# Kernel optimization log

Hardware: AMD Instinct MI355X
Metric: run time of the kernel (lower is better)

## Reference

```python
import jax, jax.numpy as jnp
import numpy as np

P, L = 4, 2                      # meta-paths, sub-layers
N_NODES, N_EDGES = 100000, 1600000
E_TABLE = 200000                 # global edge-feature table rows
D_IN = D_OUT = 128
D_META, NREG = 64, 50000
SCALE = np.float32(1.0 / np.sqrt(D_OUT))


def setup_inputs() -> dict:
    key = jax.random.key(0)
    ks = jax.random.split(key, 8)
    E = jax.random.normal(ks[0], (E_TABLE, D_IN), jnp.float32)
    metapath_emb = jax.random.normal(ks[1], (P, D_META), jnp.float32)
    W_root = jax.random.normal(ks[2], (P, L, D_IN, D_OUT), jnp.float32) * 0.05
    W_rel = jax.random.normal(ks[3], (P, L, D_IN, D_OUT), jnp.float32) * 0.05
    b = jnp.zeros((P, L, D_OUT), jnp.float32)
    Wq = jax.random.normal(ks[4], (D_META, D_OUT), jnp.float32) * 0.05
    bq = jnp.zeros((D_OUT,), jnp.float32)
    edge_index = jax.random.randint(ks[5], (P, 2, N_EDGES), 0, N_NODES, dtype=jnp.int64)
    eids = jax.random.randint(ks[6], (P, N_NODES), 0, E_TABLE, dtype=jnp.int64)
    return dict(E=E, metapath_emb=metapath_emb, W_root=W_root, W_rel=W_rel, b=b,
                Wq=Wq, bq=bq, edge_index=edge_index, eids=eids)


def _rgcn(x, src, dst, Wr, Wm, bias):
    # PyG RGCNConv, single relation, mean aggregation:
    # h_i = mean_{j->i}(x_j @ Wm) + x_i @ Wr + bias
    msg = x[src] @ Wm                                           # [E, d_out]
    agg = jax.ops.segment_sum(msg, dst, num_segments=N_NODES)   # [N, d_out]
    cnt = jax.ops.segment_sum(jnp.ones((src.shape[0], 1), x.dtype), dst,
                              num_segments=N_NODES)
    return agg / jnp.maximum(cnt, 1.0) + x @ Wr + bias


def reference(E, metapath_emb, W_root, W_rel, b, Wq, bq, edge_index, eids):
    sems = []
    for i in range(P):                      # small fixed loop over meta-paths
        src, dst = edge_index[i, 0], edge_index[i, 1]
        x = E[eids[i]]                      # gather edge features, [N, d_in]
        for j in range(L):
            x = jax.nn.relu(_rgcn(x, src, dst, W_root[i, j], W_rel[i, j], b[i, j]))
        sems.append(x[:NREG])
    emb = jnp.stack(sems, axis=1)           # [NREG, P, d_out]
    query = metapath_emb @ Wq + bq          # [P, d_out]
    # bmm + diagonal extraction == per-(n,p) dot product
    scores = jnp.einsum('pd,npd->np', query, emb) * SCALE
    w = jax.nn.softmax(scores, axis=1)      # softmax over meta-paths
    return jnp.sum(w[:, :, None] * emb, axis=1)   # [NREG, d_out]
```

## Files before the change

kernel.cpp:

```cpp
#include <hip/hip_runtime.h>

#define N_NODES 100000
#define N_EDGES 1600000
#define E_TBL   200000
#define D       128
#define NREG    50000
#define P_MP    4
#define L_SUB   2
#define D_META  64
#define SCALE_F 0.08838834764831845f

#define BKT_SHIFT 9
#define BKT_NODES 512
#define NBKT      196
#define CSB       128
#define EPB       (N_EDGES / CSB)
#define P2N       (NBKT * CSB)

typedef __attribute__((ext_vector_type(8))) short bf16x8;
typedef __attribute__((ext_vector_type(4))) float f32x4;
typedef __attribute__((ext_vector_type(2))) float f32x2;


__device__ __forceinline__ float bf2f_lo(unsigned int u) {
    union { unsigned int i; float f; } v;
    v.i = u << 16;
    return v.f;
}
__device__ __forceinline__ float bf2f_hi(unsigned int u) {
    union { unsigned int i; float f; } v;
    v.i = u & 0xffff0000u;
    return v.f;
}
__device__ __forceinline__ unsigned int f2bf(float f) {
    union { float f; unsigned int i; } v;
    v.f = f;
    return (v.i + 0x7fffu + ((v.i >> 16) & 1u)) >> 16;
}


__global__ __launch_bounds__(256) void p1_bhist(const int* __restrict__ edge_index,
                                                int* __restrict__ tbl) {
    __shared__ int h[NBKT];
    int p = blockIdx.y, b = blockIdx.x, t = threadIdx.x;
    const int* dst = edge_index + ((size_t)p * 2 + 1) * N_EDGES;
    if (t < NBKT) h[t] = 0;
    __syncthreads();
    int e0 = b * EPB;
    for (int e = e0 + t; e < e0 + EPB; e += 256)
        atomicAdd(&h[dst[e] >> BKT_SHIFT], 1);
    __syncthreads();
    if (t < NBKT) tbl[(size_t)p * P2N + t * CSB + b] = h[t];
}

__global__ __launch_bounds__(1024) void p2_scan(const int* __restrict__ tbl,
                                                int* __restrict__ tblx,
                                                int* __restrict__ offs) {
    __shared__ int ts[1024];
    int p = blockIdx.x, t = threadIdx.x;
    const int* tp = tbl + (size_t)p * P2N;
    int* xp = tblx + (size_t)p * P2N;
    int v[25];
    int base = t * 25;
    int sum = 0;
#pragma unroll
    for (int i = 0; i < 25; ++i) {
        int idx = base + i;
        int val = (idx < P2N) ? tp[idx] : 0;
        v[i] = val;
        sum += val;
    }
    ts[t] = sum;
    __syncthreads();
    for (int o = 1; o < 1024; o <<= 1) {
        int u = (t >= o) ? ts[t - o] : 0;
        __syncthreads();
        ts[t] += u;
        __syncthreads();
    }
    int run = ts[t] - sum;
#pragma unroll
    for (int i = 0; i < 25; ++i) {
        int idx = base + i;
        if (idx < P2N) xp[idx] = run;
        run += v[i];
    }
    if (t == 0) offs[(size_t)p * (N_NODES + 1) + N_NODES] = N_EDGES;
}

__global__ __launch_bounds__(256) void p3_coarse(const int* __restrict__ edge_index,
                                                 const int* __restrict__ tblx,
                                                 uint2* __restrict__ pairs) {
    __shared__ int lcur[NBKT];
    int p = blockIdx.y, b = blockIdx.x, t = threadIdx.x;
    const int* src = edge_index + ((size_t)p * 2 + 0) * N_EDGES;
    const int* dst = edge_index + ((size_t)p * 2 + 1) * N_EDGES;
    const int* txp = tblx + (size_t)p * P2N;
    uint2* pp = pairs + (size_t)p * N_EDGES;
    if (t < NBKT) lcur[t] = txp[t * CSB + b];
    __syncthreads();
    int e0 = b * EPB;
    for (int e = e0 + t; e < e0 + EPB; e += 256) {
        int d = dst[e], s0 = src[e];
        int pos = atomicAdd(&lcur[d >> BKT_SHIFT], 1);
        pp[pos] = make_uint2((unsigned)s0, (unsigned)d);
    }
}

__global__ __launch_bounds__(256) void p4_fine(const uint2* __restrict__ pairs,
                                               const int* __restrict__ tblx,
                                               int* __restrict__ offs,
                                               int* __restrict__ ssrc) {
    __shared__ int lhist[BKT_NODES];
    __shared__ int lcur[BKT_NODES];
    __shared__ int pr[256];
    int p = blockIdx.y, b = blockIdx.x, t = threadIdx.x;
    const uint2* pp = pairs + (size_t)p * N_EDGES;
    const int* txp = tblx + (size_t)p * P2N;
    int* offp = offs + (size_t)p * (N_NODES + 1);
    int* sp = ssrc + (size_t)p * N_EDGES;
    int nbase = b << BKT_SHIFT;
    int e0 = txp[b * CSB];
    int e1 = (b + 1 < NBKT) ? txp[(b + 1) * CSB] : N_EDGES;
    lhist[t] = 0;
    lhist[t + 256] = 0;
    __syncthreads();
    for (int e = e0 + t; e < e1; e += 256)
        atomicAdd(&lhist[pp[e].y - nbase], 1);
    __syncthreads();
    int c0 = lhist[2 * t], c1 = lhist[2 * t + 1];
    int ps = c0 + c1;
    pr[t] = ps;
    __syncthreads();
    for (int o = 1; o < 256; o <<= 1) {
        int u = (t >= o) ? pr[t - o] : 0;
        __syncthreads();
        pr[t] += u;
        __syncthreads();
    }
    int ex = e0 + pr[t] - ps;
    lcur[2 * t] = ex;
    lcur[2 * t + 1] = ex + c0;
    int n0 = nbase + 2 * t;
    if (n0 < N_NODES)     offp[n0] = ex;
    if (n0 + 1 < N_NODES) offp[n0 + 1] = ex + c0;
    __syncthreads();
    for (int e = e0 + t; e < e1; e += 256) {
        uint2 q = pp[e];
        int pos = atomicAdd(&lcur[q.y - nbase], 1);
        sp[pos] = (int)q.x;
    }
}


__global__ __launch_bounds__(256) void k_gather(const float* __restrict__ Etab,
                                                const int* __restrict__ eids,
                                                unsigned short* __restrict__ x0) {
    int p = blockIdx.y;
    int i = blockIdx.x * 256 + threadIdx.x;
    int n = i >> 4, g = i & 15;
    if (n >= N_NODES) return;
    int r = eids[(size_t)p * N_NODES + n];
    const float4* srcp = (const float4*)(Etab + (size_t)r * D + g * 8);
    float4 a = srcp[0], b = srcp[1];
    uint4 o;
    o.x = f2bf(a.x) | (f2bf(a.y) << 16);
    o.y = f2bf(a.z) | (f2bf(a.w) << 16);
    o.z = f2bf(b.x) | (f2bf(b.y) << 16);
    o.w = f2bf(b.z) | (f2bf(b.w) << 16);
    *(uint4*)(x0 + ((size_t)p * N_NODES + n) * D + g * 8) = o;
}


__global__ __launch_bounds__(256) void k_wswz(const float* __restrict__ Wroot,
                                              const float* __restrict__ Wrel,
                                              unsigned short* __restrict__ wswz) {
    int gid = blockIdx.x * blockDim.x + threadIdx.x;
    if (gid >= 16 * 4 * 8 * 64) return;
    int lane = gid & 63;
    int t = (gid >> 6) & 7;
    int c = (gid >> 9) & 3;
    int mat = gid >> 11;
    int which = mat & 1;
    int pl = mat >> 1;
    const float* W = (which == 0 ? Wrel : Wroot) + (size_t)pl * D * D;
    int k0 = c * 32 + (lane >> 4) * 8;
    int n = t * 16 + (lane & 15);
    unsigned short o[8];
#pragma unroll
    for (int j = 0; j < 8; ++j) o[j] = (unsigned short)f2bf(W[(size_t)(k0 + j) * D + n]);
    *(uint4*)(wswz + ((size_t)((mat * 4 + c) * 8 + t) * 64 + lane) * 8) = *(uint4*)o;
}


__device__ __forceinline__ void acc4(uint4 r, f32x2& a01, f32x2& a23, f32x2& a45, f32x2& a67) {
    f32x2 t;
    t.x = bf2f_lo(r.x); t.y = bf2f_hi(r.x); a01 += t;
    t.x = bf2f_lo(r.y); t.y = bf2f_hi(r.y); a23 += t;
    t.x = bf2f_lo(r.z); t.y = bf2f_hi(r.z); a45 += t;
    t.x = bf2f_lo(r.w); t.y = bf2f_hi(r.w); a67 += t;
}

template <bool OUT_BF16>
__global__ __launch_bounds__(256) void k_fused(const unsigned short* __restrict__ x,
                                               const int* __restrict__ offs,
                                               const int* __restrict__ ssrc,
                                               const unsigned short* __restrict__ wswz,
                                               const float* __restrict__ bvec,
                                               void* __restrict__ outv,
                                               int layer, int out_stride) {
    __shared__ __align__(16) unsigned short srow[16 * 136];
    int p = blockIdx.y;
    int w = (int)(threadIdx.x >> 6);
    int lane = (int)(threadIdx.x & 63);
    int row0 = (int)blockIdx.x << 4;
    const int* offp = offs + (size_t)p * (N_NODES + 1);
    const int* ep = ssrc + (size_t)p * N_EDGES;
    const char* xbb = (const char*)x + (size_t)p * N_NODES * 256;
    int qb = (lane >> 4) << 2;
    unsigned lo16 = (unsigned)(lane & 15) << 4;

    for (int i = 0; i < 4; ++i) {
        int dst = row0 + w * 4 + i;
        int e0 = __builtin_amdgcn_readfirstlane(offp[dst]);
        int e1 = __builtin_amdgcn_readfirstlane(offp[dst + 1]);
        f32x2 a01 = {0.f, 0.f}, a23 = {0.f, 0.f}, a45 = {0.f, 0.f}, a67 = {0.f, 0.f};
        int e = e0;
        while (e < e1) {
            int m = min(64, e1 - e);
            int v = (lane < m) ? ep[e + lane] : 0;
            int m4 = m >> 2;
            int k = 0;
            for (; k + 4 <= m4; k += 4) {
                int i0 = __builtin_amdgcn_ds_bpermute(qb + ((k + 0) << 4), v);
                int i1 = __builtin_amdgcn_ds_bpermute(qb + ((k + 1) << 4), v);
                int i2 = __builtin_amdgcn_ds_bpermute(qb + ((k + 2) << 4), v);
                int i3 = __builtin_amdgcn_ds_bpermute(qb + ((k + 3) << 4), v);
                uint4 r0 = *(const uint4*)(xbb + ((((unsigned)i0) << 8) | lo16));
                uint4 r1 = *(const uint4*)(xbb + ((((unsigned)i1) << 8) | lo16));
                uint4 r2 = *(const uint4*)(xbb + ((((unsigned)i2) << 8) | lo16));
                uint4 r3 = *(const uint4*)(xbb + ((((unsigned)i3) << 8) | lo16));
                acc4(r0, a01, a23, a45, a67);
                acc4(r1, a01, a23, a45, a67);
                acc4(r2, a01, a23, a45, a67);
                acc4(r3, a01, a23, a45, a67);
            }
            for (; k < m4; ++k) {
                int i0 = __builtin_amdgcn_ds_bpermute(qb + (k << 4), v);
                uint4 r0 = *(const uint4*)(xbb + ((((unsigned)i0) << 8) | lo16));
                acc4(r0, a01, a23, a45, a67);
            }
            int rem = m & 3;
            if (rem) {
                int iv = __builtin_amdgcn_ds_bpermute(qb + (m4 << 4), v);
                if ((lane >> 4) < rem) {
                    uint4 r = *(const uint4*)(xbb + ((((unsigned)iv) << 8) | lo16));
                    acc4(r, a01, a23, a45, a67);
                }
            }
            e += m;
        }
#pragma unroll
        for (int o = 32; o >= 16; o >>= 1) {
            f32x2 t;
            t.x = __shfl_xor(a01.x, o, 64); t.y = __shfl_xor(a01.y, o, 64); a01 += t;
            t.x = __shfl_xor(a23.x, o, 64); t.y = __shfl_xor(a23.y, o, 64); a23 += t;
            t.x = __shfl_xor(a45.x, o, 64); t.y = __shfl_xor(a45.y, o, 64); a45 += t;
            t.x = __shfl_xor(a67.x, o, 64); t.y = __shfl_xor(a67.y, o, 64); a67 += t;
        }
        int deg = e1 - e0;
        float inv = 1.0f / (float)(deg > 0 ? deg : 1);
        if (lane < 16) {
            uint4 o4;
            o4.x = f2bf(a01.x * inv) | (f2bf(a01.y * inv) << 16);
            o4.y = f2bf(a23.x * inv) | (f2bf(a23.y * inv) << 16);
            o4.z = f2bf(a45.x * inv) | (f2bf(a45.y * inv) << 16);
            o4.w = f2bf(a67.x * inv) | (f2bf(a67.y * inv) << 16);
            *(uint4*)((char*)srow + (w * 4 + i) * 272 + lo16) = o4;
        }
    }
    __syncthreads();

    const unsigned short* wm = wswz + (size_t)((p * L_SUB + layer) * 2 + 0) * D * D;
    const unsigned short* wr = wswz + (size_t)((p * L_SUB + layer) * 2 + 1) * D * D;
    const float* bias = bvec + (size_t)(p * L_SUB + layer) * D;
    int rl = lane & 15;
    int asub = (lane >> 4) * 8;
    const unsigned short* xrow = x + (size_t)p * N_NODES * D + (size_t)(row0 + rl) * D;

    union U { uint4 u; bf16x8 v; };
    f32x4 acc0 = (f32x4){0.f, 0.f, 0.f, 0.f};
    f32x4 acc1 = (f32x4){0.f, 0.f, 0.f, 0.f};
    int t0 = w * 2;
#pragma unroll
    for (int c = 0; c < 4; ++c) {
        U as, ax;
        as.u = *(const uint4*)((const char*)srow + rl * 272 + c * 64 + ((lane >> 4) << 4));
        ax.u = *(const uint4*)(xrow + c * 32 + asub);
        U b0m, b0r, b1m, b1r;
        b0m.u = *(const uint4*)(wm + ((size_t)((c * 8 + t0) * 64) + lane) * 8);
        b0r.u = *(const uint4*)(wr + ((size_t)((c * 8 + t0) * 64) + lane) * 8);
        b1m.u = *(const uint4*)(wm + ((size_t)((c * 8 + t0 + 1) * 64) + lane) * 8);
        b1r.u = *(const uint4*)(wr + ((size_t)((c * 8 + t0 + 1) * 64) + lane) * 8);
        acc0 = __builtin_amdgcn_mfma_f32_16x16x32_bf16(as.v, b0m.v, acc0, 0, 0, 0);
        acc0 = __builtin_amdgcn_mfma_f32_16x16x32_bf16(ax.v, b0r.v, acc0, 0, 0, 0);
        acc1 = __builtin_amdgcn_mfma_f32_16x16x32_bf16(as.v, b1m.v, acc1, 0, 0, 0);
        acc1 = __builtin_amdgcn_mfma_f32_16x16x32_bf16(ax.v, b1r.v, acc1, 0, 0, 0);
    }

    int rq = (lane >> 4) * 4;
#pragma unroll
    for (int tt = 0; tt < 2; ++tt) {
        f32x4 a = tt ? acc1 : acc0;
        int col = (t0 + tt) * 16 + rl;
        float bv = bias[col];
#pragma unroll
        for (int r = 0; r < 4; ++r) {
            float v = fmaxf(a[r] + bv, 0.f);
            size_t off = ((size_t)p * out_stride + row0 + rq + r) * D + col;
            if (OUT_BF16) ((unsigned short*)outv)[off] = (unsigned short)f2bf(v);
            else          ((float*)outv)[off] = v;
        }
    }
}


__global__ void k_query(const float* __restrict__ meta, const float* __restrict__ Wq,
                        const float* __restrict__ bq, float* __restrict__ query) {
    int t = blockIdx.x * blockDim.x + threadIdx.x;
    if (t < P_MP * D) {
        int p = t >> 7, c = t & 127;
        float acc = bq[c];
        for (int k = 0; k < D_META; ++k) acc += meta[p * D_META + k] * Wq[k * D + c];
        query[t] = acc;
    }
}


__global__ __launch_bounds__(256) void k_final(const float* __restrict__ emb,
                                               const float* __restrict__ query,
                                               float* __restrict__ out) {
    int wv = (blockIdx.x * blockDim.x + threadIdx.x) >> 6;
    int lane = threadIdx.x & 63;
    if (wv >= NREG) return;
    float2 e[4];
    float sc[4];
#pragma unroll
    for (int p = 0; p < 4; ++p) {
        e[p] = *(const float2*)(emb + ((size_t)p * NREG + wv) * D + lane * 2);
        float2 q = *(const float2*)(query + p * D + lane * 2);
        float d = e[p].x * q.x + e[p].y * q.y;
#pragma unroll
        for (int o = 32; o > 0; o >>= 1) d += __shfl_xor(d, o, 64);
        sc[p] = d * SCALE_F;
    }
    float mx = fmaxf(fmaxf(sc[0], sc[1]), fmaxf(sc[2], sc[3]));
    float w[4], sum = 0.f;
#pragma unroll
    for (int p = 0; p < 4; ++p) { w[p] = __expf(sc[p] - mx); sum += w[p]; }
    float inv = 1.f / sum;
    float ox = 0.f, oy = 0.f;
#pragma unroll
    for (int p = 0; p < 4; ++p) { ox += w[p] * inv * e[p].x; oy += w[p] * inv * e[p].y; }
    float2 o; o.x = ox; o.y = oy;
    *(float2*)(out + (size_t)wv * D + lane * 2) = o;
}


extern "C" void kernel_launch(void* const* d_in, const int* in_sizes, int n_in,
                              void* d_out, int out_size, void* d_ws, size_t ws_size,
                              hipStream_t stream) {
    const float* Etab  = (const float*)d_in[0];
    const float* meta  = (const float*)d_in[1];
    const float* Wroot = (const float*)d_in[2];
    const float* Wrel  = (const float*)d_in[3];
    const float* bvec  = (const float*)d_in[4];
    const float* Wq    = (const float*)d_in[5];
    const float* bq    = (const float*)d_in[6];
    const int* edge_index = (const int*)d_in[7];
    const int* eids       = (const int*)d_in[8];
    float* out = (float*)d_out;

    char* w = (char*)d_ws;
    char* regionA = w;                           w += (size_t)P_MP * N_NODES * D * 2;
    unsigned short* h1   = (unsigned short*)w;   w += (size_t)P_MP * N_NODES * D * 2;
    int* ssrc = (int*)w;                         w += (size_t)P_MP * N_EDGES * 4;
    int* offs = (int*)w;                         w += (size_t)P_MP * (N_NODES + 1) * 4 + 240;
    int* tbl  = (int*)w;                         w += (size_t)P_MP * P2N * 4;
    int* tblx = (int*)w;                         w += (size_t)P_MP * P2N * 4;
    unsigned short* wswz = (unsigned short*)w;   w += (size_t)16 * D * D * 2;
    float* query = (float*)w;                    w += 4096;

    uint2* pairs       = (uint2*)regionA;
    unsigned short* x0 = (unsigned short*)regionA;
    float* emb         = (float*)regionA;

    k_wswz<<<128, 256, 0, stream>>>(Wroot, Wrel, wswz);
    k_query<<<2, 256, 0, stream>>>(meta, Wq, bq, query);

    p1_bhist<<<dim3(CSB, P_MP), 256, 0, stream>>>(edge_index, tbl);
    p2_scan<<<dim3(P_MP), 1024, 0, stream>>>(tbl, tblx, offs);
    p3_coarse<<<dim3(CSB, P_MP), 256, 0, stream>>>(edge_index, tblx, pairs);
    p4_fine<<<dim3(NBKT, P_MP), 256, 0, stream>>>(pairs, tblx, offs, ssrc);

    k_gather<<<dim3(N_NODES * 16 / 256, P_MP), 256, 0, stream>>>(Etab, eids, x0);

    k_fused<true><<<dim3(N_NODES / 16, P_MP), 256, 0, stream>>>(
        x0, offs, ssrc, wswz, bvec, h1, 0, N_NODES);

    k_fused<false><<<dim3(NREG / 16, P_MP), 256, 0, stream>>>(
        h1, offs, ssrc, wswz, bvec, emb, 1, NREG);

    k_final<<<(NREG * 64) / 256, 256, 0, stream>>>(emb, query, out);
}
```

Before: 843.3 us.

## Gather layer-0 features through composed edge ids and fuse final attention into layer 2

Removes the per-path gather kernel: the edge table is converted once to bf16, and p4_fine writes composed indices (eids[src]) so layer 0 reads rows straight from the shared bf16 table. The second layer now loops over all four meta-paths in one block, keeps the fp32 embeddings in LDS, and does the softmax attention combine in place. This drops the emb round-trip and k_final. The cost is an extra seids array write, conversion of the full 200k-row table, and a layer-2 grid four times smaller with a larger LDS footprint.

Result: slower. 975.4 us (+15.7%).

```diff
diff --git a/kernel.cpp b/kernel.cpp
--- a/kernel.cpp
+++ b/kernel.cpp
@@ -107,18 +107,23 @@
     }
 }
 
+
 __global__ __launch_bounds__(256) void p4_fine(const uint2* __restrict__ pairs,
                                                const int* __restrict__ tblx,
+                                               const int* __restrict__ eids,
                                                int* __restrict__ offs,
-                                               int* __restrict__ ssrc) {
+                                               int* __restrict__ ssrc,
+                                               int* __restrict__ seids) {
     __shared__ int lhist[BKT_NODES];
     __shared__ int lcur[BKT_NODES];
     __shared__ int pr[256];
     int p = blockIdx.y, b = blockIdx.x, t = threadIdx.x;
     const uint2* pp = pairs + (size_t)p * N_EDGES;
     const int* txp = tblx + (size_t)p * P2N;
+    const int* eid = eids + (size_t)p * N_NODES;
     int* offp = offs + (size_t)p * (N_NODES + 1);
     int* sp = ssrc + (size_t)p * N_EDGES;
+    int* sd = seids + (size_t)p * N_EDGES;
     int nbase = b << BKT_SHIFT;
     int e0 = txp[b * CSB];
     int e1 = (b + 1 < NBKT) ? txp[(b + 1) * CSB] : N_EDGES;
@@ -149,26 +154,24 @@
         uint2 q = pp[e];
         int pos = atomicAdd(&lcur[q.y - nbase], 1);
         sp[pos] = (int)q.x;
-    }
-}
-
-
-__global__ __launch_bounds__(256) void k_gather(const float* __restrict__ Etab,
-                                                const int* __restrict__ eids,
-                                                unsigned short* __restrict__ x0) {
-    int p = blockIdx.y;
+        sd[pos] = eid[q.x];
+    }
+}
+
+
+__global__ __launch_bounds__(256) void k_ecvt(const float* __restrict__ Etab,
+                                              unsigned short* __restrict__ Eb) {
     int i = blockIdx.x * 256 + threadIdx.x;
     int n = i >> 4, g = i & 15;
-    if (n >= N_NODES) return;
-    int r = eids[(size_t)p * N_NODES + n];
-    const float4* srcp = (const float4*)(Etab + (size_t)r * D + g * 8);
-    float4 a = srcp[0], b = srcp[1];
+    if (n >= E_TBL) return;
+    const float4* s = (const float4*)(Etab + (size_t)n * D + g * 8);
+    float4 a = s[0], b = s[1];
     uint4 o;
     o.x = f2bf(a.x) | (f2bf(a.y) << 16);
     o.y = f2bf(a.z) | (f2bf(a.w) << 16);
     o.z = f2bf(b.x) | (f2bf(b.y) << 16);
     o.w = f2bf(b.z) | (f2bf(b.w) << 16);
-    *(uint4*)(x0 + ((size_t)p * N_NODES + n) * D + g * 8) = o;
+    *(uint4*)(Eb + (size_t)n * D + g * 8) = o;
 }
 
 
@@ -201,22 +204,81 @@
     t.x = bf2f_lo(r.w); t.y = bf2f_hi(r.w); a67 += t;
 }
 
-template <bool OUT_BF16>
-__global__ __launch_bounds__(256) void k_fused(const unsigned short* __restrict__ x,
-                                               const int* __restrict__ offs,
-                                               const int* __restrict__ ssrc,
-                                               const unsigned short* __restrict__ wswz,
-                                               const float* __restrict__ bvec,
-                                               void* __restrict__ outv,
-                                               int layer, int out_stride) {
+__device__ __forceinline__ void agg_row(const char* xbb, const int* ep, int e0, int e1,
+                                        int lane, int qb, unsigned lo16,
+                                        unsigned short* srow, int sidx) {
+    f32x2 a01 = {0.f, 0.f}, a23 = {0.f, 0.f}, a45 = {0.f, 0.f}, a67 = {0.f, 0.f};
+    int e = e0;
+    while (e < e1) {
+        int m = min(64, e1 - e);
+        int v = (lane < m) ? ep[e + lane] : 0;
+        int m4 = m >> 2;
+        int k = 0;
+        for (; k + 4 <= m4; k += 4) {
+            int i0 = __builtin_amdgcn_ds_bpermute(qb + ((k + 0) << 4), v);
+            int i1 = __builtin_amdgcn_ds_bpermute(qb + ((k + 1) << 4), v);
+            int i2 = __builtin_amdgcn_ds_bpermute(qb + ((k + 2) << 4), v);
+            int i3 = __builtin_amdgcn_ds_bpermute(qb + ((k + 3) << 4), v);
+            uint4 r0 = *(const uint4*)(xbb + ((size_t)(unsigned)i0 << 8) + lo16);
+            uint4 r1 = *(const uint4*)(xbb + ((size_t)(unsigned)i1 << 8) + lo16);
+            uint4 r2 = *(const uint4*)(xbb + ((size_t)(unsigned)i2 << 8) + lo16);
+            uint4 r3 = *(const uint4*)(xbb + ((size_t)(unsigned)i3 << 8) + lo16);
+            acc4(r0, a01, a23, a45, a67);
+            acc4(r1, a01, a23, a45, a67);
+            acc4(r2, a01, a23, a45, a67);
+            acc4(r3, a01, a23, a45, a67);
+        }
+        for (; k < m4; ++k) {
+            int i0 = __builtin_amdgcn_ds_bpermute(qb + (k << 4), v);
+            uint4 r0 = *(const uint4*)(xbb + ((size_t)(unsigned)i0 << 8) + lo16);
+            acc4(r0, a01, a23, a45, a67);
+        }
+        int rem = m & 3;
+        if (rem) {
+            int iv = __builtin_amdgcn_ds_bpermute(qb + (m4 << 4), v);
+            if ((lane >> 4) < rem) {
+                uint4 r = *(const uint4*)(xbb + ((size_t)(unsigned)iv << 8) + lo16);
+                acc4(r, a01, a23, a45, a67);
+            }
+        }
+        e += m;
+    }
+#pragma unroll
+    for (int o = 32; o >= 16; o >>= 1) {
+        f32x2 t;
+        t.x = __shfl_xor(a01.x, o, 64); t.y = __shfl_xor(a01.y, o, 64); a01 += t;
+        t.x = __shfl_xor(a23.x, o, 64); t.y = __shfl_xor(a23.y, o, 64); a23 += t;
+        t.x = __shfl_xor(a45.x, o, 64); t.y = __shfl_xor(a45.y, o, 64); a45 += t;
+        t.x = __shfl_xor(a67.x, o, 64); t.y = __shfl_xor(a67.y, o, 64); a67 += t;
+    }
+    int deg = e1 - e0;
+    float inv = 1.0f / (float)(deg > 0 ? deg : 1);
+    if (lane < 16) {
+        uint4 o4;
+        o4.x = f2bf(a01.x * inv) | (f2bf(a01.y * inv) << 16);
+        o4.y = f2bf(a23.x * inv) | (f2bf(a23.y * inv) << 16);
+        o4.z = f2bf(a45.x * inv) | (f2bf(a45.y * inv) << 16);
+        o4.w = f2bf(a67.x * inv) | (f2bf(a67.y * inv) << 16);
+        *(uint4*)((char*)srow + sidx * 272 + lo16) = o4;
+    }
+}
+
+
+__global__ __launch_bounds__(256) void k_fused1(const unsigned short* __restrict__ Eb,
+                                                const int* __restrict__ eids,
+                                                const int* __restrict__ offs,
+                                                const int* __restrict__ seids,
+                                                const unsigned short* __restrict__ wswz,
+                                                const float* __restrict__ bvec,
+                                                unsigned short* __restrict__ h1) {
     __shared__ __align__(16) unsigned short srow[16 * 136];
     int p = blockIdx.y;
     int w = (int)(threadIdx.x >> 6);
     int lane = (int)(threadIdx.x & 63);
     int row0 = (int)blockIdx.x << 4;
     const int* offp = offs + (size_t)p * (N_NODES + 1);
-    const int* ep = ssrc + (size_t)p * N_EDGES;
-    const char* xbb = (const char*)x + (size_t)p * N_NODES * 256;
+    const int* ep = seids + (size_t)p * N_EDGES;
+    const char* xbb = (const char*)Eb;
     int qb = (lane >> 4) << 2;
     unsigned lo16 = (unsigned)(lane & 15) << 4;
 
@@ -224,69 +286,17 @@
         int dst = row0 + w * 4 + i;
         int e0 = __builtin_amdgcn_readfirstlane(offp[dst]);
         int e1 = __builtin_amdgcn_readfirstlane(offp[dst + 1]);
-        f32x2 a01 = {0.f, 0.f}, a23 = {0.f, 0.f}, a45 = {0.f, 0.f}, a67 = {0.f, 0.f};
-        int e = e0;
-        while (e < e1) {
-            int m = min(64, e1 - e);
-            int v = (lane < m) ? ep[e + lane] : 0;
-            int m4 = m >> 2;
-            int k = 0;
-            for (; k + 4 <= m4; k += 4) {
-                int i0 = __builtin_amdgcn_ds_bpermute(qb + ((k + 0) << 4), v);
-                int i1 = __builtin_amdgcn_ds_bpermute(qb + ((k + 1) << 4), v);
-                int i2 = __builtin_amdgcn_ds_bpermute(qb + ((k + 2) << 4), v);
-                int i3 = __builtin_amdgcn_ds_bpermute(qb + ((k + 3) << 4), v);
-                uint4 r0 = *(const uint4*)(xbb + ((((unsigned)i0) << 8) | lo16));
-                uint4 r1 = *(const uint4*)(xbb + ((((unsigned)i1) << 8) | lo16));
-                uint4 r2 = *(const uint4*)(xbb + ((((unsigned)i2) << 8) | lo16));
-                uint4 r3 = *(const uint4*)(xbb + ((((unsigned)i3) << 8) | lo16));
-                acc4(r0, a01, a23, a45, a67);
-                acc4(r1, a01, a23, a45, a67);
-                acc4(r2, a01, a23, a45, a67);
-                acc4(r3, a01, a23, a45, a67);
-            }
-            for (; k < m4; ++k) {
-                int i0 = __builtin_amdgcn_ds_bpermute(qb + (k << 4), v);
-                uint4 r0 = *(const uint4*)(xbb + ((((unsigned)i0) << 8) | lo16));
-                acc4(r0, a01, a23, a45, a67);
-            }
-            int rem = m & 3;
-            if (rem) {
-                int iv = __builtin_amdgcn_ds_bpermute(qb + (m4 << 4), v);
-                if ((lane >> 4) < rem) {
-                    uint4 r = *(const uint4*)(xbb + ((((unsigned)iv) << 8) | lo16));
-                    acc4(r, a01, a23, a45, a67);
-                }
-            }
-            e += m;
-        }
-#pragma unroll
-        for (int o = 32; o >= 16; o >>= 1) {
-            f32x2 t;
-            t.x = __shfl_xor(a01.x, o, 64); t.y = __shfl_xor(a01.y, o, 64); a01 += t;
-            t.x = __shfl_xor(a23.x, o, 64); t.y = __shfl_xor(a23.y, o, 64); a23 += t;
-            t.x = __shfl_xor(a45.x, o, 64); t.y = __shfl_xor(a45.y, o, 64); a45 += t;
-            t.x = __shfl_xor(a67.x, o, 64); t.y = __shfl_xor(a67.y, o, 64); a67 += t;
-        }
-        int deg = e1 - e0;
-        float inv = 1.0f / (float)(deg > 0 ? deg : 1);
-        if (lane < 16) {
-            uint4 o4;
-            o4.x = f2bf(a01.x * inv) | (f2bf(a01.y * inv) << 16);
-            o4.y = f2bf(a23.x * inv) | (f2bf(a23.y * inv) << 16);
-            o4.z = f2bf(a45.x * inv) | (f2bf(a45.y * inv) << 16);
-            o4.w = f2bf(a67.x * inv) | (f2bf(a67.y * inv) << 16);
-            *(uint4*)((char*)srow + (w * 4 + i) * 272 + lo16) = o4;
-        }
-    }
-    __syncthreads();
-
-    const unsigned short* wm = wswz + (size_t)((p * L_SUB + layer) * 2 + 0) * D * D;
-    const unsigned short* wr = wswz + (size_t)((p * L_SUB + layer) * 2 + 1) * D * D;
-    const float* bias = bvec + (size_t)(p * L_SUB + layer) * D;
+        agg_row(xbb, ep, e0, e1, lane, qb, lo16, srow, w * 4 + i);
+    }
+    __syncthreads();
+
+    const unsigned short* wm = wswz + (size_t)((p * L_SUB + 0) * 2 + 0) * D * D;
+    const unsigned short* wr = wswz + (size_t)((p * L_SUB + 0) * 2 + 1) * D * D;
+    const float* bias = bvec + (size_t)(p * L_SUB + 0) * D;
     int rl = lane & 15;
     int asub = (lane >> 4) * 8;
-    const unsigned short* xrow = x + (size_t)p * N_NODES * D + (size_t)(row0 + rl) * D;
+    int rid = eids[(size_t)p * N_NODES + row0 + rl];
+    const unsigned short* xrow = Eb + (size_t)rid * D;
 
     union U { uint4 u; bf16x8 v; };
     f32x4 acc0 = (f32x4){0.f, 0.f, 0.f, 0.f};
@@ -317,10 +327,105 @@
 #pragma unroll
         for (int r = 0; r < 4; ++r) {
             float v = fmaxf(a[r] + bv, 0.f);
-            size_t off = ((size_t)p * out_stride + row0 + rq + r) * D + col;
-            if (OUT_BF16) ((unsigned short*)outv)[off] = (unsigned short)f2bf(v);
-            else          ((float*)outv)[off] = v;
-        }
+            h1[((size_t)p * N_NODES + row0 + rq + r) * D + col] = (unsigned short)f2bf(v);
+        }
+    }
+}
+
+
+__global__ __launch_bounds__(256) void k_fused2(const unsigned short* __restrict__ h1,
+                                                const int* __restrict__ offs,
+                                                const int* __restrict__ ssrc,
+                                                const unsigned short* __restrict__ wswz,
+                                                const float* __restrict__ bvec,
+                                                const float* __restrict__ query,
+                                                float* __restrict__ out) {
+    __shared__ __align__(16) unsigned short srow[16 * 136];
+    __shared__ float embL[P_MP][16][D];
+    int w = (int)(threadIdx.x >> 6);
+    int lane = (int)(threadIdx.x & 63);
+    int row0 = (int)blockIdx.x << 4;
+    int qb = (lane >> 4) << 2;
+    unsigned lo16 = (unsigned)(lane & 15) << 4;
+    int rl = lane & 15;
+    int asub = (lane >> 4) * 8;
+    int rq = (lane >> 4) * 4;
+    int t0 = w * 2;
+    union U { uint4 u; bf16x8 v; };
+
+    for (int p = 0; p < P_MP; ++p) {
+        const int* offp = offs + (size_t)p * (N_NODES + 1);
+        const int* ep = ssrc + (size_t)p * N_EDGES;
+        const char* xbb = (const char*)h1 + (size_t)p * N_NODES * 256;
+
+        for (int i = 0; i < 4; ++i) {
+            int dst = row0 + w * 4 + i;
+            int e0 = __builtin_amdgcn_readfirstlane(offp[dst]);
+            int e1 = __builtin_amdgcn_readfirstlane(offp[dst + 1]);
+            agg_row(xbb, ep, e0, e1, lane, qb, lo16, srow, w * 4 + i);
+        }
+        __syncthreads();
+
+        const unsigned short* wm = wswz + (size_t)((p * L_SUB + 1) * 2 + 0) * D * D;
+        const unsigned short* wr = wswz + (size_t)((p * L_SUB + 1) * 2 + 1) * D * D;
+        const float* bias = bvec + (size_t)(p * L_SUB + 1) * D;
+        const unsigned short* xrow = h1 + ((size_t)p * N_NODES + row0 + rl) * D;
+
+        f32x4 acc0 = (f32x4){0.f, 0.f, 0.f, 0.f};
+        f32x4 acc1 = (f32x4){0.f, 0.f, 0.f, 0.f};
+#pragma unroll
+        for (int c = 0; c < 4; ++c) {
+            U as, ax;
+            as.u = *(const uint4*)((const char*)srow + rl * 272 + c * 64 + ((lane >> 4) << 4));
+            ax.u = *(const uint4*)(xrow + c * 32 + asub);
+            U b0m, b0r, b1m, b1r;
+            b0m.u = *(const uint4*)(wm + ((size_t)((c * 8 + t0) * 64) + lane) * 8);
+            b0r.u = *(const uint4*)(wr + ((size_t)((c * 8 + t0) * 64) + lane) * 8);
+            b1m.u = *(const uint4*)(wm + ((size_t)((c * 8 + t0 + 1) * 64) + lane) * 8);
+            b1r.u = *(const uint4*)(wr + ((size_t)((c * 8 + t0 + 1) * 64) + lane) * 8);
+            acc0 = __builtin_amdgcn_mfma_f32_16x16x32_bf16(as.v, b0m.v, acc0, 0, 0, 0);
+            acc0 = __builtin_amdgcn_mfma_f32_16x16x32_bf16(ax.v, b0r.v, acc0, 0, 0, 0);
+            acc1 = __builtin_amdgcn_mfma_f32_16x16x32_bf16(as.v, b1m.v, acc1, 0, 0, 0);
+            acc1 = __builtin_amdgcn_mfma_f32_16x16x32_bf16(ax.v, b1r.v, acc1, 0, 0, 0);
+        }
+
+#pragma unroll
+        for (int tt = 0; tt < 2; ++tt) {
+            f32x4 a = tt ? acc1 : acc0;
+            int col = (t0 + tt) * 16 + rl;
+            float bv = bias[col];
+#pragma unroll
+            for (int r = 0; r < 4; ++r)
+                embL[p][rq + r][col] = fmaxf(a[r] + bv, 0.f);
+        }
+        __syncthreads();
+    }
+
+    for (int rr = 0; rr < 4; ++rr) {
+        int r = w * 4 + rr;
+        int node = row0 + r;
+        float2 e[P_MP];
+        float sc[P_MP];
+#pragma unroll
+        for (int p = 0; p < P_MP; ++p) {
+            e[p].x = embL[p][r][lane * 2];
+            e[p].y = embL[p][r][lane * 2 + 1];
+            float2 q = *(const float2*)(query + p * D + lane * 2);
+            float d = e[p].x * q.x + e[p].y * q.y;
+#pragma unroll
+            for (int o = 32; o > 0; o >>= 1) d += __shfl_xor(d, o, 64);
+            sc[p] = d * SCALE_F;
+        }
+        float mx = fmaxf(fmaxf(sc[0], sc[1]), fmaxf(sc[2], sc[3]));
+        float wgt[P_MP], sum = 0.f;
+#pragma unroll
+        for (int p = 0; p < P_MP; ++p) { wgt[p] = __expf(sc[p] - mx); sum += wgt[p]; }
+        float inv = 1.f / sum;
+        float ox = 0.f, oy = 0.f;
+#pragma unroll
+        for (int p = 0; p < P_MP; ++p) { ox += wgt[p] * inv * e[p].x; oy += wgt[p] * inv * e[p].y; }
+        float2 o; o.x = ox; o.y = oy;
+        *(float2*)(out + (size_t)node * D + lane * 2) = o;
     }
 }
 
@@ -334,36 +439,6 @@
         for (int k = 0; k < D_META; ++k) acc += meta[p * D_META + k] * Wq[k * D + c];
         query[t] = acc;
     }
-}
-
-
-__global__ __launch_bounds__(256) void k_final(const float* __restrict__ emb,
-                                               const float* __restrict__ query,
-                                               float* __restrict__ out) {
-    int wv = (blockIdx.x * blockDim.x + threadIdx.x) >> 6;
-    int lane = threadIdx.x & 63;
-    if (wv >= NREG) return;
-    float2 e[4];
-    float sc[4];
-#pragma unroll
-    for (int p = 0; p < 4; ++p) {
-        e[p] = *(const float2*)(emb + ((size_t)p * NREG + wv) * D + lane * 2);
-        float2 q = *(const float2*)(query + p * D + lane * 2);
-        float d = e[p].x * q.x + e[p].y * q.y;
-#pragma unroll
-        for (int o = 32; o > 0; o >>= 1) d += __shfl_xor(d, o, 64);
-        sc[p] = d * SCALE_F;
-    }
-    float mx = fmaxf(fmaxf(sc[0], sc[1]), fmaxf(sc[2], sc[3]));
-    float w[4], sum = 0.f;
-#pragma unroll
-    for (int p = 0; p < 4; ++p) { w[p] = __expf(sc[p] - mx); sum += w[p]; }
-    float inv = 1.f / sum;
-    float ox = 0.f, oy = 0.f;
-#pragma unroll
-    for (int p = 0; p < 4; ++p) { ox += w[p] * inv * e[p].x; oy += w[p] * inv * e[p].y; }
-    float2 o; o.x = ox; o.y = oy;
-    *(float2*)(out + (size_t)wv * D + lane * 2) = o;
 }
 
 
@@ -383,33 +458,30 @@
 
     char* w = (char*)d_ws;
     char* regionA = w;                           w += (size_t)P_MP * N_NODES * D * 2;
-    unsigned short* h1   = (unsigned short*)w;   w += (size_t)P_MP * N_NODES * D * 2;
-    int* ssrc = (int*)w;                         w += (size_t)P_MP * N_EDGES * 4;
-    int* offs = (int*)w;                         w += (size_t)P_MP * (N_NODES + 1) * 4 + 240;
-    int* tbl  = (int*)w;                         w += (size_t)P_MP * P2N * 4;
-    int* tblx = (int*)w;                         w += (size_t)P_MP * P2N * 4;
+    unsigned short* Eb = (unsigned short*)w;     w += (size_t)E_TBL * D * 2;
+    int* ssrc  = (int*)w;                        w += (size_t)P_MP * N_EDGES * 4;
+    int* seids = (int*)w;                        w += (size_t)P_MP * N_EDGES * 4;
+    int* offs  = (int*)w;                        w += (size_t)P_MP * (N_NODES + 1) * 4 + 240;
+    int* tbl   = (int*)w;                        w += (size_t)P_MP * P2N * 4;
+    int* tblx  = (int*)w;                        w += (size_t)P_MP * P2N * 4;
     unsigned short* wswz = (unsigned short*)w;   w += (size_t)16 * D * D * 2;
     float* query = (float*)w;                    w += 4096;
 
     uint2* pairs       = (uint2*)regionA;
-    unsigned short* x0 = (unsigned short*)regionA;
-    float* emb         = (float*)regionA;
+    unsigned short* h1 = (unsigned short*)regionA;
 
     k_wswz<<<128, 256, 0, stream>>>(Wroot, Wrel, wswz);
     k_query<<<2, 256, 0, stream>>>(meta, Wq, bq, query);
+    k_ecvt<<<(E_TBL * 16) / 256, 256, 0, stream>>>(Etab, Eb);
 
     p1_bhist<<<dim3(CSB, P_MP), 256, 0, stream>>>(edge_index, tbl);
     p2_scan<<<dim3(P_MP), 1024, 0, stream>>>(tbl, tblx, offs);
     p3_coarse<<<dim3(CSB, P_MP), 256, 0, stream>>>(edge_index, tblx, pairs);
-    p4_fine<<<dim3(NBKT, P_MP), 256, 0, stream>>>(pairs, tblx, offs, ssrc);
-
-    k_gather<<<dim3(N_NODES * 16 / 256, P_MP), 256, 0, stream>>>(Etab, eids, x0);
-
-    k_fused<true><<<dim3(N_NODES / 16, P_MP), 256, 0, stream>>>(
-        x0, offs, ssrc, wswz, bvec, h1, 0, N_NODES);
-
-    k_fused<false><<<dim3(NREG / 16, P_MP), 256, 0, stream>>>(
-        h1, offs, ssrc, wswz, bvec, emb, 1, NREG);
-
-    k_final<<<(NREG * 64) / 256, 256, 0, stream>>>(emb, query, out);
-}
+    p4_fine<<<dim3(NBKT, P_MP), 256, 0, stream>>>(pairs, tblx, eids, offs, ssrc, seids);
+
+    k_fused1<<<dim3(N_NODES / 16, P_MP), 256, 0, stream>>>(
+        Eb, eids, offs, seids, wswz, bvec, h1);
+
+    k_fused2<<<dim3(NREG / 16), 256, 0, stream>>>(
+        h1, offs, ssrc, wswz, bvec, query, out);
+}
```
